# Kernel tuning notes

Measured on AMD Instinct MI355X. Metric: run time of the kernel, lower is better.

Reference implementation:

```python
import jax, jax.numpy as jnp
import numpy as np
import math

D, NH, HD, L, P = 256, 8, 32, 4, 4
SS = np.array([[128, 128], [64, 64], [32, 32], [16, 16]], dtype=np.int32)   # (H, W) per level
LSI = np.array([0, 16384, 20480, 21504], dtype=np.int32)
N_TOTAL, B, Q = 21760, 8, 1000


def setup_inputs() -> dict:
    key = jax.random.key(0)
    ks = jax.random.split(key, 10)
    s = 0.02
    # directional bias as in the torch init (cos/sin per head, tiled over levels/points)
    thetas = jnp.arange(NH, dtype=jnp.float32) * (2.0 * math.pi / NH)
    grid = jnp.stack([jnp.cos(thetas), jnp.sin(thetas)], axis=-1)            # [NH,2]
    b_off = jnp.broadcast_to(grid[:, None, None, :], (NH, L, P, 2)).reshape(-1)
    return {
        'query': jax.random.normal(ks[0], (Q, B, D), jnp.float32),
        'reference_points': jax.random.uniform(ks[1], (Q, B, 2), jnp.float32),
        'value': jax.random.normal(ks[2], (N_TOTAL, B, D), jnp.float32),
        'spatial_shapes': jnp.asarray(SS),
        'level_start_idx': jnp.asarray(LSI),
        'W_v': jax.random.normal(ks[3], (D, D), jnp.float32) * s,
        'b_v': jnp.zeros((D,), jnp.float32),
        'W_off': jax.random.normal(ks[4], (D, NH * L * P * 2), jnp.float32) * s,
        'b_off': b_off,
        'W_attn': jax.random.normal(ks[5], (D, NH * L * P), jnp.float32) * s,
        'b_attn': jnp.zeros((NH * L * P,), jnp.float32),
        'W_out': jax.random.normal(ks[6], (D, D), jnp.float32) * s,
        'b_out': jnp.zeros((D,), jnp.float32),
    }


def _msda_forward(query, reference_points, value, ss, lsi,
                  W_v, b_v, W_off, b_off, W_attn, b_attn, W_out, b_out):
    Qn, Bn, _ = query.shape
    # value projection -> [B, N, NH, HD]
    v = (value @ W_v + b_v).transpose(1, 0, 2).reshape(Bn, -1, NH, HD)
    q = query.transpose(1, 0, 2)                                             # [B,Q,D]
    off = (q @ W_off + b_off).reshape(Bn, Qn, NH, L, P, 2)
    aw = jax.nn.softmax((q @ W_attn + b_attn).reshape(Bn, Qn, NH, L * P), axis=-1)
    aw = aw.reshape(Bn, Qn, NH, L, P)
    ref = reference_points.transpose(1, 0, 2)                                # [B,Q,2]
    ss_f = ss.astype(np.float32)
    norm = np.stack([ss_f[:, 1], ss_f[:, 0]], axis=-1)                       # (W,H) per level, [L,2]
    loc = ref[:, :, None, None, None, :] + off / (jnp.asarray(norm)[None, None, None, :, None, :] + 1e-6)
    loc = jnp.clip(loc, 0.0, 1.0)                                            # [B,Q,NH,L,P,2]

    bi = jnp.arange(Bn)[:, None, None, None]
    hi = jnp.arange(NH)[None, None, :, None]
    out = jnp.zeros((Bn, Qn, NH, HD), query.dtype)
    for lvl in range(L):
        H, W = int(ss[lvl, 0]), int(ss[lvl, 1])
        start = int(lsi[lvl])
        vf = v[:, start:start + H * W].transpose(0, 2, 1, 3)                 # [B,NH,H*W,HD]
        g = loc[:, :, :, lvl] * 2.0 - 1.0                                    # [B,Q,NH,P,2]
        # grid_sample align_corners=False pixel coords
        x = (g[..., 0] + 1.0) * (W * 0.5) - 0.5
        y = (g[..., 1] + 1.0) * (H * 0.5) - 0.5
        x0 = jnp.floor(x); y0 = jnp.floor(y)
        wx1 = x - x0; wy1 = y - y0
        x0i = x0.astype(jnp.int32); y0i = y0.astype(jnp.int32)
        samp = jnp.zeros(x.shape + (HD,), query.dtype)
        for dx, wx in ((0, 1.0 - wx1), (1, wx1)):
            for dy, wy in ((0, 1.0 - wy1), (1, wy1)):
                xi = x0i + dx; yi = y0i + dy
                valid = (xi >= 0) & (xi < W) & (yi >= 0) & (yi < H)          # zero padding
                idx = jnp.clip(yi, 0, H - 1) * W + jnp.clip(xi, 0, W - 1)
                corner = vf[bi, hi, idx]                                     # [B,Q,NH,P,HD]
                samp = samp + corner * (wx * wy * valid)[..., None]
        out = out + (samp * aw[:, :, :, lvl, :, None]).sum(axis=3)
    out = out.reshape(Bn, Qn, D) @ W_out + b_out
    return out.transpose(1, 0, 2)                                            # [Q,B,D]


def reference(query, reference_points, value, spatial_shapes, level_start_idx,
              W_v, b_v, W_off, b_off, W_attn, b_attn, W_out, b_out):
    ss = np.asarray(jax.device_get(spatial_shapes))
    lsi = np.asarray(jax.device_get(level_start_idx))
    return _msda_forward(query, reference_points, value, ss, lsi,
                         W_v, b_v, W_off, b_off, W_attn, b_attn, W_out, b_out)
```

## Files before the change

kernel.cpp:

```cpp
#include <hip/hip_runtime.h>
#include <math.h>

#define QQ     1000
#define BBATCH 8
#define NTOT   21760

typedef __bf16 bf16x8 __attribute__((ext_vector_type(8)));
typedef float  f32x4  __attribute__((ext_vector_type(4)));

__device__ __forceinline__ unsigned short bf_hi(float f, float* rem) {
    unsigned u = __builtin_bit_cast(unsigned, f);
    unsigned r = (u + 0x7FFFu + ((u >> 16) & 1u)) >> 16;
    float hf = __builtin_bit_cast(float, r << 16);
    *rem = f - hf;
    return (unsigned short)r;
}
__device__ __forceinline__ unsigned short bf_rn(float f) {
    unsigned u = __builtin_bit_cast(unsigned, f);
    return (unsigned short)((u + 0x7FFFu + ((u >> 16) & 1u)) >> 16);
}

__global__ __launch_bounds__(256) void conv_wv(
    const float* __restrict__ Wv,
    unsigned short* __restrict__ Bh, unsigned short* __restrict__ Bl)
{
    const int tid = threadIdx.x;
    const int n   = blockIdx.x * 8 + (tid >> 5);
    const int oct = tid & 31;
    const int k0  = oct * 8;
    float r0, r1, r2, r3, r4, r5, r6, r7;
    const unsigned h0 = bf_hi(Wv[(k0+0)*256 + n], &r0);
    const unsigned h1 = bf_hi(Wv[(k0+1)*256 + n], &r1);
    const unsigned h2 = bf_hi(Wv[(k0+2)*256 + n], &r2);
    const unsigned h3 = bf_hi(Wv[(k0+3)*256 + n], &r3);
    const unsigned h4 = bf_hi(Wv[(k0+4)*256 + n], &r4);
    const unsigned h5 = bf_hi(Wv[(k0+5)*256 + n], &r5);
    const unsigned h6 = bf_hi(Wv[(k0+6)*256 + n], &r6);
    const unsigned h7 = bf_hi(Wv[(k0+7)*256 + n], &r7);
    uint4 hv, lv;
    hv.x = h0 | (h1 << 16); hv.y = h2 | (h3 << 16);
    hv.z = h4 | (h5 << 16); hv.w = h6 | (h7 << 16);
    lv.x = (unsigned)bf_rn(r0) | ((unsigned)bf_rn(r1) << 16);
    lv.y = (unsigned)bf_rn(r2) | ((unsigned)bf_rn(r3) << 16);
    lv.z = (unsigned)bf_rn(r4) | ((unsigned)bf_rn(r5) << 16);
    lv.w = (unsigned)bf_rn(r6) | ((unsigned)bf_rn(r7) << 16);
    const int c  = oct >> 3;
    const int sp = (oct & 7) ^ (n & 7);
    const size_t byte = (size_t)n * 512 + (size_t)c * 128 + (size_t)sp * 16;
    *reinterpret_cast<uint4*>((char*)Bh + byte) = hv;
    *reinterpret_cast<uint4*>((char*)Bl + byte) = lv;
}

__global__ __launch_bounds__(256, 2) void gemm_value_mfma(
    const float* __restrict__ A,
    const unsigned short* __restrict__ Bth, const unsigned short* __restrict__ Btl,
    const float* __restrict__ bias, float* __restrict__ C)
{
    __shared__ unsigned short Ah_lds[64 * 64];
    __shared__ unsigned short Al_lds[64 * 64];
    __shared__ unsigned short Bh_lds[256 * 64];
    __shared__ unsigned short Bl_lds[256 * 64];

    const int tid  = threadIdx.x;
    const int lane = tid & 63;
    const int w    = tid >> 6;
    const int m0   = blockIdx.x * 64;

    f32x4 acc[4][4];
#pragma unroll
    for (int i = 0; i < 4; ++i)
#pragma unroll
        for (int j = 0; j < 4; ++j) acc[i][j] = (f32x4){0.f, 0.f, 0.f, 0.f};

    for (int kc = 0; kc < 256; kc += 64) {
        __syncthreads();
#pragma unroll
        for (int u = 0; u < 4; ++u) {
            const int idx = tid + u * 256;
            const int row = idx >> 4;
            const int c4  = (idx & 15) * 4;
            const float4 av = *reinterpret_cast<const float4*>(
                &A[(size_t)(m0 + row) * 256 + kc + c4]);
            float r0, r1, r2, r3;
            const unsigned e0 = bf_hi(av.x, &r0);
            const unsigned e1 = bf_hi(av.y, &r1);
            const unsigned e2 = bf_hi(av.z, &r2);
            const unsigned e3 = bf_hi(av.w, &r3);
            uint2 hp, lp;
            hp.x = e0 | (e1 << 16);
            hp.y = e2 | (e3 << 16);
            lp.x = (unsigned)bf_rn(r0) | ((unsigned)bf_rn(r1) << 16);
            lp.y = (unsigned)bf_rn(r2) | ((unsigned)bf_rn(r3) << 16);
            const unsigned byte = (unsigned)(row * 128 + c4 * 2) ^ ((unsigned)(row & 7) << 4);
            *reinterpret_cast<uint2*>((char*)Ah_lds + byte) = hp;
            *reinterpret_cast<uint2*>((char*)Al_lds + byte) = lp;
        }
        {
            const int r8 = lane >> 3, sl = lane & 7;
#pragma unroll
            for (int i = 0; i < 16; ++i) {
                const int chunk = w * 16 + i;
                const int plane = chunk >> 5;
                const int crow  = (chunk & 31) * 8;
                const unsigned short* gb = plane ? Btl : Bth;
                const size_t gbyte = (size_t)(crow + r8) * 512 + (size_t)kc * 2 + (size_t)sl * 16;
                unsigned short* lbase = (plane ? Bl_lds : Bh_lds) + crow * 64;
                __builtin_amdgcn_global_load_lds(
                    (const __attribute__((address_space(1))) void*)((const char*)gb + gbyte),
                    (__attribute__((address_space(3))) void*)lbase,
                    16, 0, 0);
            }
        }
        __syncthreads();
#pragma unroll
        for (int kk = 0; kk < 2; ++kk) {
            bf16x8 ah[4], al[4], bh[4], bl[4];
            const int slot = kk * 4 + (lane >> 4);
#pragma unroll
            for (int fr = 0; fr < 4; ++fr) {
                const int row = fr * 16 + (lane & 15);
                const unsigned byte = (unsigned)(row * 128) + ((unsigned)(slot ^ (row & 7)) << 4);
                ah[fr] = *reinterpret_cast<const bf16x8*>((const char*)Ah_lds + byte);
                al[fr] = *reinterpret_cast<const bf16x8*>((const char*)Al_lds + byte);
            }
#pragma unroll
            for (int fc = 0; fc < 4; ++fc) {
                const int n = w * 64 + fc * 16 + (lane & 15);
                const unsigned byte = (unsigned)(n * 128) + ((unsigned)(slot ^ (n & 7)) << 4);
                bh[fc] = *reinterpret_cast<const bf16x8*>((const char*)Bh_lds + byte);
                bl[fc] = *reinterpret_cast<const bf16x8*>((const char*)Bl_lds + byte);
            }
#pragma unroll
            for (int fr = 0; fr < 4; ++fr)
#pragma unroll
                for (int fc = 0; fc < 4; ++fc) {
                    acc[fr][fc] = __builtin_amdgcn_mfma_f32_16x16x32_bf16(ah[fr], bh[fc], acc[fr][fc], 0, 0, 0);
                    acc[fr][fc] = __builtin_amdgcn_mfma_f32_16x16x32_bf16(al[fr], bh[fc], acc[fr][fc], 0, 0, 0);
                    acc[fr][fc] = __builtin_amdgcn_mfma_f32_16x16x32_bf16(ah[fr], bl[fc], acc[fr][fc], 0, 0, 0);
                }
        }
    }
#pragma unroll
    for (int fc = 0; fc < 4; ++fc) {
        const int col = w * 64 + fc * 16 + (lane & 15);
        const float bv = bias[col];
#pragma unroll
        for (int fr = 0; fr < 4; ++fr)
#pragma unroll
            for (int ri = 0; ri < 4; ++ri) {
                const int gr = m0 + fr * 16 + (lane >> 4) * 4 + ri;
                const int orow = (gr & 7) * NTOT + (gr >> 3);
                C[(size_t)orow * 256 + col] = acc[fr][fc][ri] + bv;
            }
    }
}

template<int TM, int TN>
__global__ __launch_bounds__(256) void gemm_bias_k256(
    const float* __restrict__ A, const float* __restrict__ Bw,
    const float* __restrict__ bias, float* __restrict__ C,
    const int M, const int N, const int rmod, const int rmul)
{
    constexpr int TK = 16;
    constexpr int GM = TM / 64;
    constexpr int GN = TN / 64;
    constexpr int MM = GM * 4;
    constexpr int MN = GN * 4;
    constexpr int LDA = TM + 4;
    constexpr int LDB = TN + 4;

    __shared__ float As[TK][LDA];
    __shared__ float Bs[TK][LDB];

    const int tid = threadIdx.x;
    const int tx = tid & 15;
    const int ty = tid >> 4;
    const int m0 = blockIdx.x * TM;
    const int n0 = blockIdx.y * TN;

    float acc[MM][MN];
#pragma unroll
    for (int i = 0; i < MM; ++i)
#pragma unroll
        for (int j = 0; j < MN; ++j) acc[i][j] = 0.f;

    constexpr int LA = TM / 64;
    constexpr int LB = TN / 64;
    constexpr int B4PR = TN / 4;

    for (int kc = 0; kc < 256; kc += TK) {
        __syncthreads();
#pragma unroll
        for (int u = 0; u < LA; ++u) {
            const int idx = tid + u * 256;
            const int row = idx >> 2;
            const int c4  = (idx & 3) * 4;
            const float4 av = *reinterpret_cast<const float4*>(
                &A[(size_t)(m0 + row) * 256 + kc + c4]);
            As[c4 + 0][row] = av.x;
            As[c4 + 1][row] = av.y;
            As[c4 + 2][row] = av.z;
            As[c4 + 3][row] = av.w;
        }
#pragma unroll
        for (int u = 0; u < LB; ++u) {
            const int idx = tid + u * 256;
            const int row = idx / B4PR;
            const int c4  = (idx % B4PR) * 4;
            const float4 bv = *reinterpret_cast<const float4*>(
                &Bw[(size_t)(kc + row) * N + n0 + c4]);
            *reinterpret_cast<float4*>(&Bs[row][c4]) = bv;
        }
        __syncthreads();
#pragma unroll
        for (int k = 0; k < TK; ++k) {
            float a[MM], b[MN];
#pragma unroll
            for (int g = 0; g < GM; ++g) {
                const float4 v = *reinterpret_cast<const float4*>(&As[k][ty * 4 + g * 64]);
                a[g*4+0] = v.x; a[g*4+1] = v.y; a[g*4+2] = v.z; a[g*4+3] = v.w;
            }
#pragma unroll
            for (int g = 0; g < GN; ++g) {
                const float4 v = *reinterpret_cast<const float4*>(&Bs[k][tx * 4 + g * 64]);
                b[g*4+0] = v.x; b[g*4+1] = v.y; b[g*4+2] = v.z; b[g*4+3] = v.w;
            }
#pragma unroll
            for (int i = 0; i < MM; ++i)
#pragma unroll
                for (int j = 0; j < MN; ++j)
                    acc[i][j] = fmaf(a[i], b[j], acc[i][j]);
        }
    }

#pragma unroll
    for (int gi = 0; gi < GM; ++gi)
#pragma unroll
        for (int ii = 0; ii < 4; ++ii) {
            const int gr = m0 + ty * 4 + gi * 64 + ii;
            const int orow = (gr % rmod) * rmul + gr / rmod;
#pragma unroll
            for (int gj = 0; gj < GN; ++gj) {
                const int col = n0 + tx * 4 + gj * 64;
                float4 o;
                o.x = acc[gi*4+ii][gj*4+0] + bias[col + 0];
                o.y = acc[gi*4+ii][gj*4+1] + bias[col + 1];
                o.z = acc[gi*4+ii][gj*4+2] + bias[col + 2];
                o.w = acc[gi*4+ii][gj*4+3] + bias[col + 3];
                *reinterpret_cast<float4*>(&C[(size_t)orow * N + col]) = o;
            }
        }
}

__global__ __launch_bounds__(256) void msda_sample(
    const float* __restrict__ vproj, const float* __restrict__ off_raw,
    const float* __restrict__ attn_raw, const float* __restrict__ refp,
    float* __restrict__ tmp)
{
    const int lane = threadIdx.x & 63;
    const int widx = blockIdx.x * 4 + (threadIdx.x >> 6);
    const int h  = widx & 7;
    const int bq = widx >> 3;
    const int b  = bq / QQ;
    const int qi = bq - b * QQ;
    const int row_q = qi * BBATCH + b;

    const int s0 = lane & 15;
    const int l0 = s0 >> 2;
    float a = attn_raw[row_q * 128 + h * 16 + s0];
    float m = a;
#pragma unroll
    for (int msk = 8; msk >= 1; msk >>= 1) m = fmaxf(m, __shfl_xor(m, msk));
    const float e = __expf(a - m);
    float ssum = e;
#pragma unroll
    for (int msk = 8; msk >= 1; msk >>= 1) ssum += __shfl_xor(ssum, msk);
    const float wv = e / ssum;

    const float offx = off_raw[row_q * 256 + (h * 16 + s0) * 2 + 0];
    const float offy = off_raw[row_q * 256 + (h * 16 + s0) * 2 + 1];
    const float rx = refp[row_q * 2 + 0];
    const float ry = refp[row_q * 2 + 1];
    const float Wf = (float)(128 >> l0);
    float lx = rx + offx / (Wf + 1e-6f);
    float ly = ry + offy / (Wf + 1e-6f);
    lx = fminf(fmaxf(lx, 0.f), 1.f);
    ly = fminf(fmaxf(ly, 0.f), 1.f);
    const float xv = lx * Wf - 0.5f;
    const float yv = ly * Wf - 0.5f;

    const int c = lane & 31;
    const int sbase = (lane >> 5) * 8;
    const float* __restrict__ vb = vproj + (size_t)b * NTOT * 256 + h * 32 + c;

    float acc = 0.f;
#pragma unroll
    for (int i = 0; i < 8; ++i) {
        const int s = sbase + i;
        const float xs = __shfl(xv, s);
        const float ys = __shfl(yv, s);
        const float ws = __shfl(wv, s);
        const int l = s >> 2;
        const int Wl = 128 >> l;
        const int start = (65536 - (65536 >> (2 * l))) / 3;
        const float x0f = floorf(xs), y0f = floorf(ys);
        const float fx = xs - x0f, fy = ys - y0f;
        const int x0 = (int)x0f, y0 = (int)y0f;
        const int x1 = x0 + 1,   y1 = y0 + 1;
        const float vx0 = (x0 >= 0 && x0 < Wl) ? 1.f : 0.f;
        const float vx1 = (x1 >= 0 && x1 < Wl) ? 1.f : 0.f;
        const float vy0 = (y0 >= 0 && y0 < Wl) ? 1.f : 0.f;
        const float vy1 = (y1 >= 0 && y1 < Wl) ? 1.f : 0.f;
        const int xc0 = min(max(x0, 0), Wl - 1);
        const int xc1 = min(max(x1, 0), Wl - 1);
        const int yc0 = min(max(y0, 0), Wl - 1);
        const int yc1 = min(max(y1, 0), Wl - 1);
        const float* base = vb + (size_t)start * 256;
        const float v00 = base[(size_t)(yc0 * Wl + xc0) * 256];
        const float v10 = base[(size_t)(yc0 * Wl + xc1) * 256];
        const float v01 = base[(size_t)(yc1 * Wl + xc0) * 256];
        const float v11 = base[(size_t)(yc1 * Wl + xc1) * 256];
        const float w00 = (1.f - fx) * (1.f - fy) * vx0 * vy0;
        const float w10 = fx * (1.f - fy) * vx1 * vy0;
        const float w01 = (1.f - fx) * fy * vx0 * vy1;
        const float w11 = fx * fy * vx1 * vy1;
        acc += ws * (w00 * v00 + w10 * v10 + w01 * v01 + w11 * v11);
    }
    acc += __shfl_xor(acc, 32);
    if (lane < 32) tmp[(size_t)bq * 256 + h * 32 + c] = acc;
}

extern "C" void kernel_launch(void* const* d_in, const int* in_sizes, int n_in,
                              void* d_out, int out_size, void* d_ws, size_t ws_size,
                              hipStream_t stream) {
    (void)in_sizes; (void)n_in; (void)out_size; (void)ws_size;

    const float* query  = (const float*)d_in[0];
    const float* refp   = (const float*)d_in[1];
    const float* value  = (const float*)d_in[2];
    const float* W_v    = (const float*)d_in[5];
    const float* b_v    = (const float*)d_in[6];
    const float* W_off  = (const float*)d_in[7];
    const float* b_off  = (const float*)d_in[8];
    const float* W_attn = (const float*)d_in[9];
    const float* b_attn = (const float*)d_in[10];
    const float* W_out  = (const float*)d_in[11];
    const float* b_out  = (const float*)d_in[12];
    float* out = (float*)d_out;

    float* vproj    = (float*)d_ws;
    float* off_raw  = vproj + (size_t)44564480;
    float* attn_raw = off_raw + 2048000;
    float* tmp      = attn_raw + 1024000;
    unsigned short* Bt_h = (unsigned short*)tmp;
    unsigned short* Bt_l = Bt_h + 65536;

    const dim3 blk(256);
    conv_wv<<<dim3(32), blk, 0, stream>>>(W_v, Bt_h, Bt_l);
    gemm_value_mfma<<<dim3(2720), blk, 0, stream>>>(value, Bt_h, Bt_l, b_v, vproj);
    gemm_bias_k256<64,64><<<dim3(125, 4), blk, 0, stream>>>(
        query, W_off, b_off, off_raw, 8000, 256, 1 << 30, 1);
    gemm_bias_k256<64,64><<<dim3(125, 2), blk, 0, stream>>>(
        query, W_attn, b_attn, attn_raw, 8000, 128, 1 << 30, 1);
    msda_sample<<<dim3(16000), blk, 0, stream>>>(vproj, off_raw, attn_raw, refp, tmp);
    gemm_bias_k256<64,64><<<dim3(125, 4), blk, 0, stream>>>(
        tmp, W_out, b_out, out, 8000, 256, 1000, 8);
}
```

Baseline: 448.3 us.

## Replace FP32 query and output GEMMs with split-bf16 MFMA kernels, fusing offset/attn

Replaces the scalar FP32 SIMT GEMMs for the offset, attention and output projections with an MFMA kernel that splits operands into bf16 high and low parts (three MFMAs per tile) for near-FP32 accuracy. The offset and attention weight matrices are concatenated and converted once, so both projections run in a single launch that reads query once. B tiles are staged with global_load_lds. Costs are an extra weight-conversion kernel, idle waves in the partially filled column tile, and tripled MFMA work for precision.

```diff
diff --git a/kernel.cpp b/kernel.cpp
--- a/kernel.cpp
+++ b/kernel.cpp
@@ -51,6 +51,38 @@
     *reinterpret_cast<uint4*>((char*)Bl + byte) = lv;
 }
 
+__global__ __launch_bounds__(256) void conv_wcat(
+    const float* __restrict__ W_off, const float* __restrict__ W_attn,
+    const float* __restrict__ W_out,
+    unsigned short* __restrict__ Bh, unsigned short* __restrict__ Bl)
+{
+    const int tid = threadIdx.x;
+    const int n   = blockIdx.x * 8 + (tid >> 5);
+    const int oct = tid & 31;
+    const int k0  = oct * 8;
+    const float* src; int col, ld;
+    if (n < 256)      { src = W_off;  col = n;       ld = 256; }
+    else if (n < 384) { src = W_attn; col = n - 256; ld = 128; }
+    else              { src = W_out;  col = n - 384; ld = 256; }
+    unsigned hw[8], lw[8];
+#pragma unroll
+    for (int j = 0; j < 8; ++j) {
+        float r;
+        hw[j] = bf_hi(src[(size_t)(k0 + j) * ld + col], &r);
+        lw[j] = bf_rn(r);
+    }
+    uint4 hv, lv;
+    hv.x = hw[0] | (hw[1] << 16); hv.y = hw[2] | (hw[3] << 16);
+    hv.z = hw[4] | (hw[5] << 16); hv.w = hw[6] | (hw[7] << 16);
+    lv.x = lw[0] | (lw[1] << 16); lv.y = lw[2] | (lw[3] << 16);
+    lv.z = lw[4] | (lw[5] << 16); lv.w = lw[6] | (lw[7] << 16);
+    const int c  = oct >> 3;
+    const int sp = (oct & 7) ^ (n & 7);
+    const size_t byte = (size_t)n * 512 + (size_t)c * 128 + (size_t)sp * 16;
+    *reinterpret_cast<uint4*>((char*)Bh + byte) = hv;
+    *reinterpret_cast<uint4*>((char*)Bl + byte) = lv;
+}
+
 __global__ __launch_bounds__(256, 2) void gemm_value_mfma(
     const float* __restrict__ A,
     const unsigned short* __restrict__ Bth, const unsigned short* __restrict__ Btl,
@@ -155,101 +187,123 @@
     }
 }
 
-template<int TM, int TN>
-__global__ __launch_bounds__(256) void gemm_bias_k256(
-    const float* __restrict__ A, const float* __restrict__ Bw,
-    const float* __restrict__ bias, float* __restrict__ C,
-    const int M, const int N, const int rmod, const int rmul)
+template<int MODE>
+__global__ __launch_bounds__(256, 2) void gemm_q_mfma(
+    const float* __restrict__ A,
+    const unsigned short* __restrict__ Bth, const unsigned short* __restrict__ Btl,
+    const float* __restrict__ bias0, const float* __restrict__ bias1,
+    float* __restrict__ C0, float* __restrict__ C1,
+    const int N, const int rmod, const int rmul)
 {
-    constexpr int TK = 16;
-    constexpr int GM = TM / 64;
-    constexpr int GN = TN / 64;
-    constexpr int MM = GM * 4;
-    constexpr int MN = GN * 4;
-    constexpr int LDA = TM + 4;
-    constexpr int LDB = TN + 4;
-
-    __shared__ float As[TK][LDA];
-    __shared__ float Bs[TK][LDB];
-
-    const int tid = threadIdx.x;
-    const int tx = tid & 15;
-    const int ty = tid >> 4;
-    const int m0 = blockIdx.x * TM;
-    const int n0 = blockIdx.y * TN;
-
-    float acc[MM][MN];
-#pragma unroll
-    for (int i = 0; i < MM; ++i)
-#pragma unroll
-        for (int j = 0; j < MN; ++j) acc[i][j] = 0.f;
-
-    constexpr int LA = TM / 64;
-    constexpr int LB = TN / 64;
-    constexpr int B4PR = TN / 4;
-
-    for (int kc = 0; kc < 256; kc += TK) {
+    __shared__ unsigned short Ah_lds[64 * 64];
+    __shared__ unsigned short Al_lds[64 * 64];
+    __shared__ unsigned short Bh_lds[256 * 64];
+    __shared__ unsigned short Bl_lds[256 * 64];
+
+    const int tid  = threadIdx.x;
+    const int lane = tid & 63;
+    const int w    = tid >> 6;
+    const int m0   = blockIdx.x * 64;
+    const int n0   = blockIdx.y * 256;
+    const int ac   = min(256, N - n0);
+    const bool active = (w * 64) < ac;
+    const int cpw  = ac >> 4;
+    const int rpp  = ac >> 3;
+
+    f32x4 acc[4][4];
+#pragma unroll
+    for (int i = 0; i < 4; ++i)
+#pragma unroll
+        for (int j = 0; j < 4; ++j) acc[i][j] = (f32x4){0.f, 0.f, 0.f, 0.f};
+
+    for (int kc = 0; kc < 256; kc += 64) {
         __syncthreads();
 #pragma unroll
-        for (int u = 0; u < LA; ++u) {
+        for (int u = 0; u < 4; ++u) {
             const int idx = tid + u * 256;
-            const int row = idx >> 2;
-            const int c4  = (idx & 3) * 4;
+            const int row = idx >> 4;
+            const int c4  = (idx & 15) * 4;
             const float4 av = *reinterpret_cast<const float4*>(
                 &A[(size_t)(m0 + row) * 256 + kc + c4]);
-            As[c4 + 0][row] = av.x;
-            As[c4 + 1][row] = av.y;
-            As[c4 + 2][row] = av.z;
-            As[c4 + 3][row] = av.w;
-        }
-#pragma unroll
-        for (int u = 0; u < LB; ++u) {
-            const int idx = tid + u * 256;
-            const int row = idx / B4PR;
-            const int c4  = (idx % B4PR) * 4;
-            const float4 bv = *reinterpret_cast<const float4*>(
-                &Bw[(size_t)(kc + row) * N + n0 + c4]);
-            *reinterpret_cast<float4*>(&Bs[row][c4]) = bv;
+            float r0, r1, r2, r3;
+            const unsigned e0 = bf_hi(av.x, &r0);
+            const unsigned e1 = bf_hi(av.y, &r1);
+            const unsigned e2 = bf_hi(av.z, &r2);
+            const unsigned e3 = bf_hi(av.w, &r3);
+            uint2 hp, lp;
+            hp.x = e0 | (e1 << 16);
+            hp.y = e2 | (e3 << 16);
+            lp.x = (unsigned)bf_rn(r0) | ((unsigned)bf_rn(r1) << 16);
+            lp.y = (unsigned)bf_rn(r2) | ((unsigned)bf_rn(r3) << 16);
+            const unsigned byte = (unsigned)(row * 128 + c4 * 2) ^ ((unsigned)(row & 7) << 4);
+            *reinterpret_cast<uint2*>((char*)Ah_lds + byte) = hp;
+            *reinterpret_cast<uint2*>((char*)Al_lds + byte) = lp;
+        }
+        {
+            const int r8 = lane >> 3, sl = lane & 7;
+            for (int i = 0; i < cpw; ++i) {
+                const int chunk = w * cpw + i;
+                const int plane = chunk >= rpp;
+                const int crow  = (plane ? chunk - rpp : chunk) * 8;
+                const unsigned short* gb = plane ? Btl : Bth;
+                const size_t gbyte = (size_t)(n0 + crow + r8) * 512 + (size_t)kc * 2 + (size_t)sl * 16;
+                unsigned short* lbase = (plane ? Bl_lds : Bh_lds) + crow * 64;
+                __builtin_amdgcn_global_load_lds(
+                    (const __attribute__((address_space(1))) void*)((const char*)gb + gbyte),
+                    (__attribute__((address_space(3))) void*)lbase,
+                    16, 0, 0);
+            }
         }
         __syncthreads();
-#pragma unroll
-        for (int k = 0; k < TK; ++k) {
-            float a[MM], b[MN];
-#pragma unroll
-            for (int g = 0; g < GM; ++g) {
-                const float4 v = *reinterpret_cast<const float4*>(&As[k][ty * 4 + g * 64]);
-                a[g*4+0] = v.x; a[g*4+1] = v.y; a[g*4+2] = v.z; a[g*4+3] = v.w;
-            }
-#pragma unroll
-            for (int g = 0; g < GN; ++g) {
-                const float4 v = *reinterpret_cast<const float4*>(&Bs[k][tx * 4 + g * 64]);
-                b[g*4+0] = v.x; b[g*4+1] = v.y; b[g*4+2] = v.z; b[g*4+3] = v.w;
-            }
-#pragma unroll
-            for (int i = 0; i < MM; ++i)
-#pragma unroll
-                for (int j = 0; j < MN; ++j)
-                    acc[i][j] = fmaf(a[i], b[j], acc[i][j]);
-        }
-    }
-
-#pragma unroll
-    for (int gi = 0; gi < GM; ++gi)
-#pragma unroll
-        for (int ii = 0; ii < 4; ++ii) {
-            const int gr = m0 + ty * 4 + gi * 64 + ii;
-            const int orow = (gr % rmod) * rmul + gr / rmod;
-#pragma unroll
-            for (int gj = 0; gj < GN; ++gj) {
-                const int col = n0 + tx * 4 + gj * 64;
-                float4 o;
-                o.x = acc[gi*4+ii][gj*4+0] + bias[col + 0];
-                o.y = acc[gi*4+ii][gj*4+1] + bias[col + 1];
-                o.z = acc[gi*4+ii][gj*4+2] + bias[col + 2];
-                o.w = acc[gi*4+ii][gj*4+3] + bias[col + 3];
-                *reinterpret_cast<float4*>(&C[(size_t)orow * N + col]) = o;
-            }
-        }
+        if (active) {
+#pragma unroll
+            for (int kk = 0; kk < 2; ++kk) {
+                bf16x8 ah[4], al[4], bh[4], bl[4];
+                const int slot = kk * 4 + (lane >> 4);
+#pragma unroll
+                for (int fr = 0; fr < 4; ++fr) {
+                    const int row = fr * 16 + (lane & 15);
+                    const unsigned byte = (unsigned)(row * 128) + ((unsigned)(slot ^ (row & 7)) << 4);
+                    ah[fr] = *reinterpret_cast<const bf16x8*>((const char*)Ah_lds + byte);
+                    al[fr] = *reinterpret_cast<const bf16x8*>((const char*)Al_lds + byte);
+                }
+#pragma unroll
+                for (int fc = 0; fc < 4; ++fc) {
+                    const int n = w * 64 + fc * 16 + (lane & 15);
+                    const unsigned byte = (unsigned)(n * 128) + ((unsigned)(slot ^ (n & 7)) << 4);
+                    bh[fc] = *reinterpret_cast<const bf16x8*>((const char*)Bh_lds + byte);
+                    bl[fc] = *reinterpret_cast<const bf16x8*>((const char*)Bl_lds + byte);
+                }
+#pragma unroll
+                for (int fr = 0; fr < 4; ++fr)
+#pragma unroll
+                    for (int fc = 0; fc < 4; ++fc) {
+                        acc[fr][fc] = __builtin_amdgcn_mfma_f32_16x16x32_bf16(ah[fr], bh[fc], acc[fr][fc], 0, 0, 0);
+                        acc[fr][fc] = __builtin_amdgcn_mfma_f32_16x16x32_bf16(al[fr], bh[fc], acc[fr][fc], 0, 0, 0);
+                        acc[fr][fc] = __builtin_amdgcn_mfma_f32_16x16x32_bf16(ah[fr], bl[fc], acc[fr][fc], 0, 0, 0);
+                    }
+            }
+        }
+    }
+    if (!active) return;
+#pragma unroll
+    for (int fc = 0; fc < 4; ++fc) {
+        const int colg = n0 + w * 64 + fc * 16 + (lane & 15);
+#pragma unroll
+        for (int fr = 0; fr < 4; ++fr)
+#pragma unroll
+            for (int ri = 0; ri < 4; ++ri) {
+                const int gr = m0 + fr * 16 + (lane >> 4) * 4 + ri;
+                const float v = acc[fr][fc][ri];
+                if (MODE == 0) {
+                    const int orow = (gr % rmod) * rmul + gr / rmod;
+                    C0[(size_t)orow * 256 + colg] = v + bias0[colg];
+                } else {
+                    if (colg < 256) C0[(size_t)gr * 256 + colg] = v + bias0[colg];
+                    else            C1[(size_t)gr * 128 + colg - 256] = v + bias1[colg - 256];
+                }
+            }
+    }
 }
 
 __global__ __launch_bounds__(256) void msda_sample(
@@ -352,17 +406,19 @@
     float* off_raw  = vproj + (size_t)44564480;
     float* attn_raw = off_raw + 2048000;
     float* tmp      = attn_raw + 1024000;
-    unsigned short* Bt_h = (unsigned short*)tmp;
-    unsigned short* Bt_l = Bt_h + 65536;
+    unsigned short* Bt_h   = (unsigned short*)tmp;
+    unsigned short* Bt_l   = Bt_h + 65536;
+    unsigned short* Wcat_h = (unsigned short*)(tmp + 2048000);
+    unsigned short* Wcat_l = Wcat_h + 640 * 256;
 
     const dim3 blk(256);
     conv_wv<<<dim3(32), blk, 0, stream>>>(W_v, Bt_h, Bt_l);
+    conv_wcat<<<dim3(80), blk, 0, stream>>>(W_off, W_attn, W_out, Wcat_h, Wcat_l);
     gemm_value_mfma<<<dim3(2720), blk, 0, stream>>>(value, Bt_h, Bt_l, b_v, vproj);
-    gemm_bias_k256<64,64><<<dim3(125, 4), blk, 0, stream>>>(
-        query, W_off, b_off, off_raw, 8000, 256, 1 << 30, 1);
-    gemm_bias_k256<64,64><<<dim3(125, 2), blk, 0, stream>>>(
-        query, W_attn, b_attn, attn_raw, 8000, 128, 1 << 30, 1);
+    gemm_q_mfma<1><<<dim3(125, 2), blk, 0, stream>>>(
+        query, Wcat_h, Wcat_l, b_off, b_attn, off_raw, attn_raw, 384, 0, 0);
     msda_sample<<<dim3(16000), blk, 0, stream>>>(vproj, off_raw, attn_raw, refp, tmp);
-    gemm_bias_k256<64,64><<<dim3(125, 4), blk, 0, stream>>>(
-        tmp, W_out, b_out, out, 8000, 256, 1000, 8);
-}
+    gemm_q_mfma<0><<<dim3(125, 1), blk, 0, stream>>>(
+        tmp, Wcat_h + 384 * 256, Wcat_l + 384 * 256, b_out, nullptr,
+        out, nullptr, 256, 1000, 8);
+}
```

Measured after the change: 433.2 us. 3.4% less time.
